# Kernel optimization log

Hardware: AMD Instinct MI355X
Metric: run time of the kernel (lower is better)

## Reference

```python
import jax, jax.numpy as jnp
import numpy as np

WALL, SRC_REAL, SRC_IMAG, DELAY_REAL, DELAY_IMAG = 0, 1, 2, 3, 4
DELAY_STEP = 8
MAX_PHASE_NORM = 2.0
READOUT_THRESHOLD = 0.35
PHASE_CLASSES = 8


def conv2d(x, w, b, pad):
    y = jax.lax.conv_general_dilated(x, w, (1, 1), [(pad, pad), (pad, pad)],
                                     dimension_numbers=('NCHW', 'OIHW', 'NCHW'))
    return y + b[None, :, None, None]


def clamp_phase(r, i):
    mag = jnp.sqrt(r * r + i * i + 1e-8)
    s = jnp.minimum(MAX_PHASE_NORM / mag, 1.0)
    return r * s, i * s


def neighbor_sum(x):
    # zero-padded 4-neighbor shift-and-sum stencil
    p = jnp.pad(x, ((0, 0), (0, 0), (1, 1), (1, 1)))
    return (p[:, :, 2:, 1:-1] + p[:, :, :-2, 1:-1] +
            p[:, :, 1:-1, 2:] + p[:, :, 1:-1, :-2])


def setup_inputs() -> dict:
    key = jax.random.key(0)
    ks = jax.random.split(key, 8)
    B, H, W, WD = 8, 256, 256, 32
    CIN = 6 + 4  # INPUT_CHANNELS + 4 (state_r, state_i, frontier_r, frontier_i)
    x = jax.random.normal(ks[0], (B, 6, H, W), jnp.float32)
    target = jax.random.randint(ks[1], (B, 2), 0, H)
    w_in = jax.random.normal(ks[2], (WD, CIN, 1, 1), jnp.float32) * (1.0 / np.sqrt(CIN))
    b_in = jnp.zeros((WD,), jnp.float32)
    w_up = jax.random.normal(ks[3], (WD, WD + CIN, 3, 3), jnp.float32) * (1.0 / np.sqrt((WD + CIN) * 9))
    b_up = jnp.zeros((WD,), jnp.float32)
    w_gate = jax.random.normal(ks[4], (1, WD + CIN, 1, 1), jnp.float32) * (1.0 / np.sqrt(WD + CIN))
    b_gate = jnp.zeros((1,), jnp.float32)
    angle = jnp.float32(0.0)
    decay_logit = jnp.float32(3.9)
    return dict(x=x, target=target, w_in=w_in, b_in=b_in, w_up=w_up, b_up=b_up,
                w_gate=w_gate, b_gate=b_gate, angle=angle, decay_logit=decay_logit, steps=16)


def reference(x, target, w_in, b_in, w_up, b_up, w_gate, b_gate, angle, decay_logit, steps):
    wall = x[:, WALL:WALL + 1]
    free = 1.0 - wall
    state_r = x[:, SRC_REAL:SRC_REAL + 1] * free
    state_i = x[:, SRC_IMAG:SRC_IMAG + 1] * free
    frontier_r, frontier_i = state_r, state_i
    h = jnp.tanh(conv2d(jnp.concatenate([x, state_r, state_i, frontier_r, frontier_i], 1), w_in, b_in, 0)) * free

    ang = jnp.tanh(angle) * 0.02
    cos_a, sin_a = jnp.cos(ang), jnp.sin(ang)
    decay = 0.95 + 0.05 * jax.nn.sigmoid(decay_logit)
    delay_r = x[:, DELAY_REAL:DELAY_REAL + 1]
    delay_i = x[:, DELAY_IMAG:DELAY_IMAG + 1]

    def body(carry, step):
        s_r, s_i, f_r, f_i, hh = carry
        inc_r = neighbor_sum(f_r)
        inc_i = neighbor_sum(f_i)
        is_delay = (step == DELAY_STEP).astype(x.dtype)
        inc_r = inc_r + is_delay * delay_r
        inc_i = inc_i + is_delay * delay_i
        source = jnp.concatenate([hh, x, s_r, s_i, f_r, f_i], 1)
        g = 0.998 + 0.002 * jax.nn.sigmoid(conv2d(source, w_gate, b_gate, 0))
        inc_r = inc_r * g
        inc_i = inc_i * g
        rot_r = inc_r * cos_a - inc_i * sin_a
        rot_i = inc_r * sin_a + inc_i * cos_a
        inc_r, inc_i = rot_r * free, rot_i * free
        inc_r, inc_i = clamp_phase(inc_r, inc_i)
        pre_wall = ((jnp.abs(inc_r) + jnp.abs(inc_i)) * wall).mean()
        s_r, s_i = clamp_phase(decay * s_r + inc_r, decay * s_i + inc_i)
        s_r = s_r * free
        s_i = s_i * free
        hh = jnp.tanh(0.8 * hh + conv2d(source, w_up, b_up, 1)) * free
        st = jnp.concatenate([s_r, s_i], 1)
        return (s_r, s_i, inc_r, inc_i, hh), (st, pre_wall)

    carry0 = (state_r, state_i, frontier_r, frontier_i, h)
    _, (sts, pre_walls) = jax.lax.scan(body, carry0, jnp.arange(1, steps + 1))
    state0 = jnp.concatenate([state_r, state_i], 1)
    states = jnp.concatenate([state0[None], sts], 0)  # [steps+1, B, 2, H, W]
    final = states[-1]

    diffs = states[1:] - states[:-1]
    delta = jnp.mean(jnp.sqrt(jnp.mean(diffs ** 2, axis=(1, 2, 3, 4))))
    norm_by_step = jnp.mean(jnp.sqrt(jnp.sum(states ** 2, axis=2)))
    sat = (jnp.abs(final) > 4.0).astype(jnp.float32).mean()
    pw = pre_walls.mean()
    norm = jnp.sqrt(jnp.sum(final ** 2, axis=1, keepdims=True))
    leak = ((norm > 0.5) & (wall > 0.5)).astype(jnp.float32).mean()
    stats = jnp.stack([delta, norm_by_step, sat, pw, leak])

    b = jnp.arange(final.shape[0])
    vec = final[b, :, target[:, 0], target[:, 1]]  # [B, 2]
    k = jnp.arange(PHASE_CLASSES)
    theta = 2.0 * jnp.pi * k / PHASE_CLASSES
    phases = jnp.stack([jnp.cos(theta), jnp.sin(theta)], axis=1)  # [K, 2]
    mag = jnp.sqrt(jnp.sum(vec ** 2, axis=1) + 1e-8)
    none = (READOUT_THRESHOLD - mag) * 12.0
    phase_logits = (vec @ phases.T - READOUT_THRESHOLD) * 12.0
    logits = jnp.concatenate([none[:, None], phase_logits], axis=1)
    return logits, stats
```

## Files before the change

### kernel.cpp

```cpp
#include <hip/hip_runtime.h>
#include <hip/hip_bf16.h>

#define HW2D 65536
#define NPIX 524288
#define NB 8
#define PW 258
#define PP 66564
#define NSTEPS 16
#define RHH 2064
#define RTT 4128
#define ROWB 8256

typedef __hip_bfloat16 bf16;
typedef unsigned long long u64;
typedef __attribute__((ext_vector_type(8))) short short8;
typedef __attribute__((ext_vector_type(4))) float f32x4;

__device__ __forceinline__ unsigned short f2bfu(float v){
  bf16 h = __float2bfloat16(v); return *(unsigned short*)&h;
}
__device__ __forceinline__ float blo(unsigned int w){ return __uint_as_float(w<<16); }
__device__ __forceinline__ float bhi(unsigned int w){ return __uint_as_float(w & 0xffff0000u); }
__device__ __forceinline__ float tanh_a(float z){
  return z*__builtin_amdgcn_rsqf(fmaf(z, z, 1.0f));
}
__device__ __forceinline__ float fast_sigmoid(float z){
  return 1.0f/(1.0f + __expf(-z));
}
__device__ __forceinline__ unsigned char f2fp8(float v){
  return (unsigned char)(__builtin_amdgcn_cvt_pk_fp8_f32(v, 0.f, 0, false) & 0xFF);
}
__device__ __forceinline__ int chmap(int m){ return (m>>1) + (m&1)*16; }

__global__ void k_prep(const float* angle, const float* decay_logit,
                       float* ST, float* PRM){
  int t = threadIdx.x;
  for (int i = t; i < 64*32; i += 256) ST[i] = 0.0f;
  if (t == 0){
    float ang = tanhf(angle[0])*0.02f;
    PRM[0] = cosf(ang);
    PRM[1] = sinf(ang);
    PRM[2] = 0.95f + 0.05f/(1.0f+expf(-decay_logit[0]));
  }
}

__global__ void k_wprep(const float* __restrict__ w_up, const float* __restrict__ w_gate,
                        u64* __restrict__ WB8, short8* __restrict__ WB16){
  int t = threadIdx.x;
  int lane = t & 63;
  int r_ = lane & 15, g = lane >> 4;
  for (int slot = t>>6; slot < 19; slot += 4){
    u64 v = 0;
    #pragma unroll
    for (int j=0;j<8;j++){
      float w = 0.f;
      int ch = chmap(g*8+j);
      if (slot < 18){
        int tile = slot/9, s = slot%9;
        int oc = tile*16 + r_;
        int dy=s/3, dx=s%3;
        w = w_up[((oc*42+ch)*3+dy)*3+dx];
        if (s==4 && oc==ch) w += 0.8f;
      } else {
        if (r_==0) w = w_gate[ch];
      }
      v |= ((u64)f2fp8(w)) << (8*j);
    }
    WB8[slot*64+lane] = v;
  }
  for (int slot = t>>6; slot < 11; slot += 4){
    short8 v;
    #pragma unroll
    for (int j=0;j<8;j++){
      float w = 0.f;
      int tt = (g&1)*8 + j;
      int tapsel = g>>1;
      if (slot < 10){
        int tile = slot/5, s2 = slot%5;
        int tap = 2*s2 + tapsel;
        int oc = tile*16 + r_;
        if (tap <= 8 && tt < 10){
          int src = (tt<4) ? (38+tt) : (32+(tt-4));
          int dy=tap/3, dx=tap%3;
          w = w_up[((oc*42+src)*3+dy)*3+dx];
        }
      } else {
        if (r_==0 && tapsel==0 && tt<10){
          int src = (tt<4) ? (38+tt) : (32+(tt-4));
          w = w_gate[src];
        }
      }
      v[j] = (short)f2bfu(w);
    }
    WB16[slot*64+lane] = v;
  }
}

__global__ void k_border(unsigned char* HH0, unsigned char* HH1,
                         unsigned char* TAIL0, unsigned char* TAIL1){
  int i = blockIdx.x*256 + threadIdx.x;
  if (i >= NB*PP) return;
  int b = i / PP, pp_ = i % PP;
  int row = pp_ / PW, col = pp_ % PW;
  if (row != 0 && row != 257 && col != 0 && col != 257) return;
  size_t rb = (size_t)(b*PW + row);
  #pragma unroll
  for (int g=0; g<4; g++){
    size_t a = (rb*4+g)*RHH + (size_t)col*8;
    *(uint2*)(HH0+a) = (uint2){0,0};
    *(uint2*)(HH1+a) = (uint2){0,0};
  }
  #pragma unroll
  for (int h=0; h<2; h++){
    size_t a = (rb*2+h)*RTT + (size_t)col*16;
    *(uint4*)(TAIL0+a) = (uint4){0,0,0,0};
    *(uint4*)(TAIL1+a) = (uint4){0,0,0,0};
  }
}

__global__ void k_init(const float* __restrict__ x, const float* __restrict__ w_in,
                       const float* __restrict__ b_in,
                       float* __restrict__ WALL,
                       unsigned char* __restrict__ HH0, unsigned char* __restrict__ TAIL0,
                       unsigned char* __restrict__ TAIL1, float* ST){
  int tid = threadIdx.x;
  int p = blockIdx.x*256 + tid;
  int b = p >> 16, rem = p & 65535;
  int y = rem >> 8, xc = rem & 255;
  const float* xb = x + (size_t)b*6*HW2D;
  float wall = xb[rem];
  float fre = 1.0f - wall;
  float s_r = xb[HW2D + rem]*fre;
  float s_i = xb[2*HW2D + rem]*fre;
  WALL[p] = wall;
  float src10[10];
  src10[0]=wall;
  #pragma unroll
  for (int c=1;c<6;c++) src10[c]=xb[c*HW2D+rem];
  src10[6]=s_r; src10[7]=s_i; src10[8]=s_r; src10[9]=s_i;
  float hv[32];
  #pragma unroll
  for (int c=0;c<32;c++){
    float a = b_in[c];
    #pragma unroll
    for (int k=0;k<10;k++) a += w_in[c*10+k]*src10[k];
    hv[c] = tanh_a(a)*fre;
  }
  unsigned int words[8];
  #pragma unroll
  for (int w=0;w<8;w++){
    int lo = __builtin_amdgcn_cvt_pk_fp8_f32(hv[2*w], hv[16+2*w], 0, false);
    words[w] = (unsigned int)__builtin_amdgcn_cvt_pk_fp8_f32(hv[2*w+1], hv[17+2*w], lo, true);
  }
  size_t rb = (size_t)(b*PW + y + 1);
  #pragma unroll
  for (int g=0; g<4; g++){
    *(uint2*)(HH0 + (rb*4+g)*RHH + (size_t)(xc+1)*8) = (uint2){words[2*g], words[2*g+1]};
  }
  unsigned short tv[16];
  tv[0]=f2bfu(s_r); tv[1]=f2bfu(s_i); tv[2]=f2bfu(s_r); tv[3]=f2bfu(s_i);
  #pragma unroll
  for (int c=0;c<6;c++) tv[4+c] = f2bfu(src10[c]);
  #pragma unroll
  for (int c=10;c<16;c++) tv[c] = 0;
  #pragma unroll
  for (int h=0; h<2; h++){
    short8 v;
    #pragma unroll
    for (int j=0;j<8;j++) v[j] = (short)tv[h*8+j];
    *(short8*)(TAIL0 + (rb*2+h)*RTT + (size_t)(xc+1)*16) = v;
    *(short8*)(TAIL1 + (rb*2+h)*RTT + (size_t)(xc+1)*16) = v;
  }
  float v = __builtin_amdgcn_sqrtf(s_r*s_r + s_i*s_i);
  #pragma unroll
  for (int off=32; off>0; off>>=1) v += __shfl_down(v, off);
  if ((tid&63)==0) atomicAdd(&ST[(blockIdx.x & 63)*32 + 16], v);
}

__global__ __launch_bounds__(256) void k_step(
    const unsigned char* __restrict__ HHo, unsigned char* __restrict__ HHn,
    const unsigned char* __restrict__ TAILo, unsigned char* __restrict__ TAILn,
    const float* __restrict__ WALL,
    const u64* __restrict__ WB8, const short8* __restrict__ WB16,
    const float* __restrict__ b_up, const float* __restrict__ x,
    const float* __restrict__ b_gate, const float* __restrict__ PRM,
    float* ST, int step){
  int bid = blockIdx.x;
  int b = bid & 7, y = bid >> 3;
  int tid = threadIdx.x;
  int wv = tid >> 6, lane = tid & 63;
  int r_ = lane & 15, g = lane >> 4;
  int px0 = wv*64 + r_;

  const unsigned char* Tc = TAILo + (size_t)(b*PW + y + 1)*ROWB + (size_t)(tid+1)*16;
  unsigned int sw  = *(const unsigned int*)(Tc);
  unsigned int fu  = *(const unsigned int*)(Tc - ROWB + 4);
  unsigned int fd  = *(const unsigned int*)(Tc + ROWB + 4);
  unsigned int fl  = *(const unsigned int*)(Tc - 16 + 4);
  unsigned int fr2 = *(const unsigned int*)(Tc + 16 + 4);
  float dlr = 0.f, dli = 0.f;
  if (step==8){
    const float* xb = x + (size_t)b*6*HW2D;
    int rem = (y<<8)+tid;
    dlr = xb[3*HW2D+rem]; dli = xb[4*HW2D+rem];
  }
  float wallB = WALL[b*HW2D + (y<<8) + tid];
  float ca = PRM[0], sa = PRM[1], dec = PRM[2];

  const unsigned char* Hrow = HHo + (size_t)(b*PW + y)*ROWB + (size_t)g*RHH + (size_t)px0*8;
  const unsigned char* Trow = TAILo + (size_t)(b*PW + y)*ROWB + (size_t)(g&1)*RTT + (size_t)px0*16;
  const unsigned char* Tzero = TAILo + (size_t)(b*PW)*ROWB + (size_t)(g&1)*RTT + (size_t)px0*16;
  int gb = g >> 1;
  const unsigned char* tb0 = Trow + (size_t)((0+gb)/3)*ROWB + (size_t)((0+gb)%3)*16;
  const unsigned char* tb1 = Trow + (size_t)((2+gb)/3)*ROWB + (size_t)((2+gb)%3)*16;
  const unsigned char* tb2 = Trow + (size_t)((4+gb)/3)*ROWB + (size_t)((4+gb)%3)*16;
  const unsigned char* tb3 = Trow + (size_t)((6+gb)/3)*ROWB + (size_t)((6+gb)%3)*16;
  const unsigned char* tb4 = gb ? Tzero : (Trow + 2*ROWB + 2*16);
  const u64* wb8l = WB8 + lane;
  const short8* wb16l = WB16 + lane;

  f32x4 acc[4][2], accg[4];
  #pragma unroll
  for (int mt=0;mt<4;mt++){
    acc[mt][0] = (f32x4){0.f,0.f,0.f,0.f};
    acc[mt][1] = (f32x4){0.f,0.f,0.f,0.f};
    accg[mt]   = (f32x4){0.f,0.f,0.f,0.f};
  }

  __builtin_amdgcn_s_setprio(1);
  #pragma unroll
  for (int s=0;s<9;s++){
    u64 b0 = wb8l[s*64], b1 = wb8l[(9+s)*64];
    u64 aH[4];
    #pragma unroll
    for (int mt=0;mt<4;mt++)
      aH[mt] = *(const u64*)(Hrow + (size_t)((s/3)*ROWB) + ((s%3)*8 + mt*128));
    #pragma unroll
    for (int mt=0;mt<4;mt++){
      acc[mt][0] = __builtin_amdgcn_mfma_f32_16x16x32_fp8_fp8((long)b0, (long)aH[mt], acc[mt][0], 0,0,0);
      acc[mt][1] = __builtin_amdgcn_mfma_f32_16x16x32_fp8_fp8((long)b1, (long)aH[mt], acc[mt][1], 0,0,0);
    }
    if (s==4){
      u64 bg = wb8l[18*64];
      #pragma unroll
      for (int mt=0;mt<4;mt++)
        accg[mt] = __builtin_amdgcn_mfma_f32_16x16x32_fp8_fp8((long)bg, (long)aH[mt], accg[mt], 0,0,0);
    }
  }
  #pragma unroll
  for (int s2=0;s2<5;s2++){
    short8 b0 = wb16l[s2*64], b1 = wb16l[(5+s2)*64];
    const unsigned char* tb = (s2==0)?tb0:(s2==1)?tb1:(s2==2)?tb2:(s2==3)?tb3:tb4;
    short8 aT[4];
    #pragma unroll
    for (int mt=0;mt<4;mt++)
      aT[mt] = *(const short8*)(tb + mt*256);
    #pragma unroll
    for (int mt=0;mt<4;mt++){
      acc[mt][0] = __builtin_amdgcn_mfma_f32_16x16x32_bf16(b0, aT[mt], acc[mt][0], 0,0,0);
      acc[mt][1] = __builtin_amdgcn_mfma_f32_16x16x32_bf16(b1, aT[mt], acc[mt][1], 0,0,0);
    }
    if (s2==2){
      short8 bgt = wb16l[10*64];
      #pragma unroll
      for (int mt=0;mt<4;mt++)
        accg[mt] = __builtin_amdgcn_mfma_f32_16x16x32_bf16(bgt, aT[mt], accg[mt], 0,0,0);
    }
  }
  __builtin_amdgcn_s_setprio(0);

  float ga0 = __shfl(accg[0][0], r_);
  float ga1 = __shfl(accg[1][0], r_);
  float ga2 = __shfl(accg[2][0], r_);
  float ga3 = __shfl(accg[3][0], r_);
  float gpre = (g==0) ? ga0 : (g==1) ? ga1 : (g==2) ? ga2 : ga3;

  const float* wallrow = WALL + (size_t)b*HW2D + (y<<8);
  const float4* bup4 = (const float4*)b_up;
  float4 bb0 = bup4[g];
  float4 bb1 = bup4[4+g];
  unsigned char* Hn = HHn + ((size_t)(b*PW + y + 1)*4 + g)*RHH;
  #pragma unroll
  for (int mt=0;mt<4;mt++){
    int px = px0 + mt*16;
    float fre = 1.0f - wallrow[px];
    float tA0 = tanh_a(acc[mt][0][0] + bb0.x)*fre;
    float tB0 = tanh_a(acc[mt][1][0] + bb1.x)*fre;
    float tA1 = tanh_a(acc[mt][0][1] + bb0.y)*fre;
    float tB1 = tanh_a(acc[mt][1][1] + bb1.y)*fre;
    float tA2 = tanh_a(acc[mt][0][2] + bb0.z)*fre;
    float tB2 = tanh_a(acc[mt][1][2] + bb1.z)*fre;
    float tA3 = tanh_a(acc[mt][0][3] + bb0.w)*fre;
    float tB3 = tanh_a(acc[mt][1][3] + bb1.w)*fre;
    int w0 = __builtin_amdgcn_cvt_pk_fp8_f32(tA0, tB0, 0, false);
    w0 = __builtin_amdgcn_cvt_pk_fp8_f32(tA1, tB1, w0, true);
    int w1 = __builtin_amdgcn_cvt_pk_fp8_f32(tA2, tB2, 0, false);
    w1 = __builtin_amdgcn_cvt_pk_fp8_f32(tA3, tB3, w1, true);
    *(uint2*)(Hn + (size_t)(px+1)*8) = (uint2){(unsigned)w0, (unsigned)w1};
  }

  float s_r = blo(sw), s_i = bhi(sw);
  float incr = blo(fu) + blo(fd) + blo(fl) + blo(fr2) + dlr;
  float inci = bhi(fu) + bhi(fd) + bhi(fl) + bhi(fr2) + dli;
  float fre = 1.0f - wallB;
  float a = gpre + b_gate[0];
  float gg = 0.998f + 0.002f*fast_sigmoid(a);
  incr *= gg; inci *= gg;
  float rr = incr*ca - inci*sa;
  float ri = incr*sa + inci*ca;
  incr = rr*fre; inci = ri*fre;
  float m1 = fmaf(incr,incr, fmaf(inci,inci, 1e-8f));
  float sc2 = fminf(2.0f*__builtin_amdgcn_rsqf(m1), 1.0f);
  incr *= sc2; inci *= sc2;
  float pw = (fabsf(incr)+fabsf(inci))*wallB;
  float nr = dec*s_r + incr, ni = dec*s_i + inci;
  float m2 = fmaf(nr,nr, fmaf(ni,ni, 1e-8f));
  sc2 = fminf(2.0f*__builtin_amdgcn_rsqf(m2), 1.0f);
  nr = nr*sc2*fre; ni = ni*sc2*fre;
  ushort4 pk;
  pk.x = f2bfu(nr); pk.y = f2bfu(ni); pk.z = f2bfu(incr); pk.w = f2bfu(inci);
  *(ushort4*)(TAILn + (size_t)(b*PW + y + 1)*ROWB + (size_t)(tid+1)*16) = pk;
  float d2 = (nr-s_r)*(nr-s_r)+(ni-s_i)*(ni-s_i);
  float nrm = __builtin_amdgcn_sqrtf(nr*nr+ni*ni);
  #pragma unroll
  for (int off=32; off>0; off>>=1){
    d2  += __shfl_down(d2, off);
    nrm += __shfl_down(nrm, off);
    pw  += __shfl_down(pw, off);
  }
  if (step==16){
    float sat = (fabsf(nr)>4.0f ? 1.0f:0.0f) + (fabsf(ni)>4.0f ? 1.0f:0.0f);
    float nn = __builtin_amdgcn_sqrtf(nr*nr+ni*ni);
    float leak = (nn>0.5f && wallB>0.5f) ? 1.0f : 0.0f;
    #pragma unroll
    for (int off=32; off>0; off>>=1){
      sat  += __shfl_down(sat, off);
      leak += __shfl_down(leak, off);
    }
    if (lane==0){
      float* st = ST + ((bid*4+wv) & 63)*32;
      atomicAdd(&st[18], sat);
      atomicAdd(&st[19], leak);
    }
  }
  if (lane==0){
    float* st = ST + ((bid*4+wv) & 63)*32;
    atomicAdd(&st[step-1], d2);
    atomicAdd(&st[16],     nrm);
    atomicAdd(&st[17],     pw);
  }
}

__global__ void k_final(const unsigned char* __restrict__ TAIL, const int* __restrict__ target,
                        const float* __restrict__ ST, float* __restrict__ out){
  int t = threadIdx.x;
  if (t < 8){
    int ty = target[2*t], tx = target[2*t+1];
    unsigned int sw = *(const unsigned int*)(TAIL + (size_t)(t*PW+ty+1)*ROWB + (size_t)(tx+1)*16);
    float vr = blo(sw), vi = bhi(sw);
    float mag = sqrtf(vr*vr+vi*vi+1e-8f);
    out[t*9] = (0.35f - mag)*12.0f;
    #pragma unroll
    for (int k=0;k<8;k++){
      float th = 6.283185307179586f * (float)k / 8.0f;
      out[t*9+1+k] = (vr*cosf(th)+vi*sinf(th) - 0.35f)*12.0f;
    }
  }
  float tot[20];
  #pragma unroll
  for (int i=0;i<20;i++){
    float v = ST[t*32 + i];
    #pragma unroll
    for (int off=32; off>0; off>>=1) v += __shfl_down(v, off);
    tot[i] = v;
  }
  if (t == 0){
    float d = 0.0f;
    #pragma unroll
    for (int s=0;s<16;s++) d += sqrtf(tot[s]/1048576.0f);
    out[72] = d/16.0f;
    out[73] = tot[16]/8912896.0f;
    out[74] = tot[18]/1048576.0f;
    out[75] = tot[17]/(524288.0f*16.0f);
    out[76] = tot[19]/524288.0f;
  }
}

extern "C" void kernel_launch(void* const* d_in, const int* in_sizes, int n_in,
                              void* d_out, int out_size, void* d_ws, size_t ws_size,
                              hipStream_t stream) {
  const float* x       = (const float*)d_in[0];
  const int*   target  = (const int*)  d_in[1];
  const float* w_in    = (const float*)d_in[2];
  const float* b_in    = (const float*)d_in[3];
  const float* w_up    = (const float*)d_in[4];
  const float* b_up    = (const float*)d_in[5];
  const float* w_gate  = (const float*)d_in[6];
  const float* b_gate  = (const float*)d_in[7];
  const float* angle   = (const float*)d_in[8];
  const float* decay_l = (const float*)d_in[9];
  float* out = (float*)d_out;

  char* ws = (char*)d_ws;
  size_t off = 0;
  unsigned char* HH0 = (unsigned char*)(ws+off); off += (size_t)NB*PP*32;
  unsigned char* HH1 = (unsigned char*)(ws+off); off += (size_t)NB*PP*32;
  unsigned char* TAIL0=(unsigned char*)(ws+off); off += (size_t)NB*PP*32;
  unsigned char* TAIL1=(unsigned char*)(ws+off); off += (size_t)NB*PP*32;
  float* WALL = (float*)(ws+off); off += (size_t)NPIX*4;
  u64* WB8 = (u64*)(ws+off); off += (size_t)19*64*8;
  short8* WB16 = (short8*)(ws+off); off += (size_t)11*64*16;
  float* ST = (float*)(ws+off); off += (size_t)64*32*4;
  float* PRM = (float*)(ws+off); off += 16*4;

  k_prep<<<1,256,0,stream>>>(angle, decay_l, ST, PRM);
  k_wprep<<<1,256,0,stream>>>(w_up, w_gate, WB8, WB16);
  k_border<<<(NB*PP+255)/256,256,0,stream>>>(HH0, HH1, TAIL0, TAIL1);
  k_init<<<NPIX/256,256,0,stream>>>(x, w_in, b_in, WALL, HH0, TAIL0, TAIL1, ST);

  unsigned char *hho=HH0, *hhn=HH1, *tlo=TAIL0, *tln=TAIL1;
  for (int t=1;t<=NSTEPS;t++){
    k_step<<<2048,256,0,stream>>>(hho, hhn, tlo, tln, WALL,
                                  WB8, WB16, b_up, x, b_gate, PRM, ST, t);
    unsigned char* tc=hho; hho=hhn; hhn=tc;
    tc=tlo; tlo=tln; tln=tc;
  }
  k_final<<<1,64,0,stream>>>(tlo, target, ST, out);
}
```

Measured before the change: 511.7 us.

## Split step GEMM into two halves to cut register pressure and raise occupancy

The per-row conv GEMM in k_step now runs in two passes over pairs of pixel tiles. Each pass keeps 6 accumulators live instead of 12 and runs its tanh/fp8 epilogue right after its MFMAs. Launch bounds also ask for 8 blocks per CU. The aim is higher occupancy and better latency hiding. The cost is that weight fragments are reloaded for each half, and less independent MFMA work is available per wave.

```diff
diff --git a/kernel.cpp b/kernel.cpp
--- a/kernel.cpp
+++ b/kernel.cpp
@@ -31,6 +31,25 @@
   return (unsigned char)(__builtin_amdgcn_cvt_pk_fp8_f32(v, 0.f, 0, false) & 0xFF);
 }
 __device__ __forceinline__ int chmap(int m){ return (m>>1) + (m&1)*16; }
+
+__device__ __forceinline__ void epilogue_mt(
+    f32x4 A, f32x4 B, float4 bb0, float4 bb1,
+    const float* __restrict__ wallrow, unsigned char* __restrict__ Hn, int px){
+  float fre = 1.0f - wallrow[px];
+  float tA0 = tanh_a(A[0] + bb0.x)*fre;
+  float tB0 = tanh_a(B[0] + bb1.x)*fre;
+  float tA1 = tanh_a(A[1] + bb0.y)*fre;
+  float tB1 = tanh_a(B[1] + bb1.y)*fre;
+  float tA2 = tanh_a(A[2] + bb0.z)*fre;
+  float tB2 = tanh_a(B[2] + bb1.z)*fre;
+  float tA3 = tanh_a(A[3] + bb0.w)*fre;
+  float tB3 = tanh_a(B[3] + bb1.w)*fre;
+  int w0 = __builtin_amdgcn_cvt_pk_fp8_f32(tA0, tB0, 0, false);
+  w0 = __builtin_amdgcn_cvt_pk_fp8_f32(tA1, tB1, w0, true);
+  int w1 = __builtin_amdgcn_cvt_pk_fp8_f32(tA2, tB2, 0, false);
+  w1 = __builtin_amdgcn_cvt_pk_fp8_f32(tA3, tB3, w1, true);
+  *(uint2*)(Hn + (size_t)(px+1)*8) = (uint2){(unsigned)w0, (unsigned)w1};
+}
 
 __global__ void k_prep(const float* angle, const float* decay_logit,
                        float* ST, float* PRM){
@@ -177,7 +196,7 @@
   if ((tid&63)==0) atomicAdd(&ST[(blockIdx.x & 63)*32 + 16], v);
 }
 
-__global__ __launch_bounds__(256) void k_step(
+__global__ __launch_bounds__(256, 8) void k_step(
     const unsigned char* __restrict__ HHo, unsigned char* __restrict__ HHn,
     const unsigned char* __restrict__ TAILo, unsigned char* __restrict__ TAILn,
     const float* __restrict__ WALL,
@@ -219,84 +238,64 @@
   const u64* wb8l = WB8 + lane;
   const short8* wb16l = WB16 + lane;
 
-  f32x4 acc[4][2], accg[4];
-  #pragma unroll
-  for (int mt=0;mt<4;mt++){
-    acc[mt][0] = (f32x4){0.f,0.f,0.f,0.f};
-    acc[mt][1] = (f32x4){0.f,0.f,0.f,0.f};
-    accg[mt]   = (f32x4){0.f,0.f,0.f,0.f};
-  }
-
-  __builtin_amdgcn_s_setprio(1);
-  #pragma unroll
-  for (int s=0;s<9;s++){
-    u64 b0 = wb8l[s*64], b1 = wb8l[(9+s)*64];
-    u64 aH[4];
-    #pragma unroll
-    for (int mt=0;mt<4;mt++)
-      aH[mt] = *(const u64*)(Hrow + (size_t)((s/3)*ROWB) + ((s%3)*8 + mt*128));
-    #pragma unroll
-    for (int mt=0;mt<4;mt++){
-      acc[mt][0] = __builtin_amdgcn_mfma_f32_16x16x32_fp8_fp8((long)b0, (long)aH[mt], acc[mt][0], 0,0,0);
-      acc[mt][1] = __builtin_amdgcn_mfma_f32_16x16x32_fp8_fp8((long)b1, (long)aH[mt], acc[mt][1], 0,0,0);
-    }
-    if (s==4){
-      u64 bg = wb8l[18*64];
-      #pragma unroll
-      for (int mt=0;mt<4;mt++)
-        accg[mt] = __builtin_amdgcn_mfma_f32_16x16x32_fp8_fp8((long)bg, (long)aH[mt], accg[mt], 0,0,0);
-    }
-  }
-  #pragma unroll
-  for (int s2=0;s2<5;s2++){
-    short8 b0 = wb16l[s2*64], b1 = wb16l[(5+s2)*64];
-    const unsigned char* tb = (s2==0)?tb0:(s2==1)?tb1:(s2==2)?tb2:(s2==3)?tb3:tb4;
-    short8 aT[4];
-    #pragma unroll
-    for (int mt=0;mt<4;mt++)
-      aT[mt] = *(const short8*)(tb + mt*256);
-    #pragma unroll
-    for (int mt=0;mt<4;mt++){
-      acc[mt][0] = __builtin_amdgcn_mfma_f32_16x16x32_bf16(b0, aT[mt], acc[mt][0], 0,0,0);
-      acc[mt][1] = __builtin_amdgcn_mfma_f32_16x16x32_bf16(b1, aT[mt], acc[mt][1], 0,0,0);
-    }
-    if (s2==2){
-      short8 bgt = wb16l[10*64];
-      #pragma unroll
-      for (int mt=0;mt<4;mt++)
-        accg[mt] = __builtin_amdgcn_mfma_f32_16x16x32_bf16(bgt, aT[mt], accg[mt], 0,0,0);
-    }
-  }
-  __builtin_amdgcn_s_setprio(0);
-
-  float ga0 = __shfl(accg[0][0], r_);
-  float ga1 = __shfl(accg[1][0], r_);
-  float ga2 = __shfl(accg[2][0], r_);
-  float ga3 = __shfl(accg[3][0], r_);
-  float gpre = (g==0) ? ga0 : (g==1) ? ga1 : (g==2) ? ga2 : ga3;
-
   const float* wallrow = WALL + (size_t)b*HW2D + (y<<8);
   const float4* bup4 = (const float4*)b_up;
   float4 bb0 = bup4[g];
   float4 bb1 = bup4[4+g];
   unsigned char* Hn = HHn + ((size_t)(b*PW + y + 1)*4 + g)*RHH;
-  #pragma unroll
-  for (int mt=0;mt<4;mt++){
-    int px = px0 + mt*16;
-    float fre = 1.0f - wallrow[px];
-    float tA0 = tanh_a(acc[mt][0][0] + bb0.x)*fre;
-    float tB0 = tanh_a(acc[mt][1][0] + bb1.x)*fre;
-    float tA1 = tanh_a(acc[mt][0][1] + bb0.y)*fre;
-    float tB1 = tanh_a(acc[mt][1][1] + bb1.y)*fre;
-    float tA2 = tanh_a(acc[mt][0][2] + bb0.z)*fre;
-    float tB2 = tanh_a(acc[mt][1][2] + bb1.z)*fre;
-    float tA3 = tanh_a(acc[mt][0][3] + bb0.w)*fre;
-    float tB3 = tanh_a(acc[mt][1][3] + bb1.w)*fre;
-    int w0 = __builtin_amdgcn_cvt_pk_fp8_f32(tA0, tB0, 0, false);
-    w0 = __builtin_amdgcn_cvt_pk_fp8_f32(tA1, tB1, w0, true);
-    int w1 = __builtin_amdgcn_cvt_pk_fp8_f32(tA2, tB2, 0, false);
-    w1 = __builtin_amdgcn_cvt_pk_fp8_f32(tA3, tB3, w1, true);
-    *(uint2*)(Hn + (size_t)(px+1)*8) = (uint2){(unsigned)w0, (unsigned)w1};
+
+  float gpre = 0.0f;
+  #pragma unroll
+  for (int half=0; half<2; half++){
+    const int mtA = half*2, mtB = half*2+1;
+    f32x4 a00 = (f32x4){0.f,0.f,0.f,0.f};
+    f32x4 a01 = (f32x4){0.f,0.f,0.f,0.f};
+    f32x4 a10 = (f32x4){0.f,0.f,0.f,0.f};
+    f32x4 a11 = (f32x4){0.f,0.f,0.f,0.f};
+    f32x4 ag0 = (f32x4){0.f,0.f,0.f,0.f};
+    f32x4 ag1 = (f32x4){0.f,0.f,0.f,0.f};
+
+    __builtin_amdgcn_s_setprio(1);
+    #pragma unroll
+    for (int s=0;s<9;s++){
+      u64 b0 = wb8l[s*64], b1 = wb8l[(9+s)*64];
+      const int aoff = (s/3)*ROWB + (s%3)*8;
+      u64 hA = *(const u64*)(Hrow + aoff + mtA*128);
+      u64 hB = *(const u64*)(Hrow + aoff + mtB*128);
+      a00 = __builtin_amdgcn_mfma_f32_16x16x32_fp8_fp8((long)b0, (long)hA, a00, 0,0,0);
+      a01 = __builtin_amdgcn_mfma_f32_16x16x32_fp8_fp8((long)b1, (long)hA, a01, 0,0,0);
+      a10 = __builtin_amdgcn_mfma_f32_16x16x32_fp8_fp8((long)b0, (long)hB, a10, 0,0,0);
+      a11 = __builtin_amdgcn_mfma_f32_16x16x32_fp8_fp8((long)b1, (long)hB, a11, 0,0,0);
+      if (s==4){
+        u64 bg = wb8l[18*64];
+        ag0 = __builtin_amdgcn_mfma_f32_16x16x32_fp8_fp8((long)bg, (long)hA, ag0, 0,0,0);
+        ag1 = __builtin_amdgcn_mfma_f32_16x16x32_fp8_fp8((long)bg, (long)hB, ag1, 0,0,0);
+      }
+    }
+    #pragma unroll
+    for (int s2=0;s2<5;s2++){
+      short8 b0 = wb16l[s2*64], b1 = wb16l[(5+s2)*64];
+      const unsigned char* tb = (s2==0)?tb0:(s2==1)?tb1:(s2==2)?tb2:(s2==3)?tb3:tb4;
+      short8 tA = *(const short8*)(tb + mtA*256);
+      short8 tB = *(const short8*)(tb + mtB*256);
+      a00 = __builtin_amdgcn_mfma_f32_16x16x32_bf16(b0, tA, a00, 0,0,0);
+      a01 = __builtin_amdgcn_mfma_f32_16x16x32_bf16(b1, tA, a01, 0,0,0);
+      a10 = __builtin_amdgcn_mfma_f32_16x16x32_bf16(b0, tB, a10, 0,0,0);
+      a11 = __builtin_amdgcn_mfma_f32_16x16x32_bf16(b1, tB, a11, 0,0,0);
+      if (s2==2){
+        short8 bgt = wb16l[10*64];
+        ag0 = __builtin_amdgcn_mfma_f32_16x16x32_bf16(bgt, tA, ag0, 0,0,0);
+        ag1 = __builtin_amdgcn_mfma_f32_16x16x32_bf16(bgt, tB, ag1, 0,0,0);
+      }
+    }
+    __builtin_amdgcn_s_setprio(0);
+
+    float gA = __shfl(ag0[0], r_);
+    float gB = __shfl(ag1[0], r_);
+    if ((g>>1) == half) gpre = (g&1) ? gB : gA;
+
+    epilogue_mt(a00, a01, bb0, bb1, wallrow, Hn, px0 + mtA*16);
+    epilogue_mt(a10, a11, bb0, bb1, wallrow, Hn, px0 + mtB*16);
   }
 
   float s_r = blo(sw), s_i = bhi(sw);
```

Measured after the change: 961.6 us. 87.9% more time.
